# Kernel tuning notes

Measured on AMD Instinct MI355X. Metric: run time of the kernel, lower is better.

The kernel has to match this reference:

```python
import jax, jax.numpy as jnp
import numpy as np

N_HOS, N_TYP, N_STRUCTS = 2, 3, 8
N_COMBOS = N_HOS * N_TYP  # 6
BATCH = 32768
N_ITERS = 150  # PDHG iterations to solve the per-sample QP

S_NP = np.array([[1,0,0,1,0,1,0,0],
                 [0,1,0,1,0,0,1,0],
                 [0,0,1,0,1,0,0,1],
                 [1,0,0,0,1,1,0,0],
                 [0,1,0,0,0,0,1,1],
                 [0,0,1,1,1,0,0,0]], dtype=np.float32)


def setup_inputs() -> dict:
    key = jax.random.key(0)
    ks = jax.random.split(key, 10)
    def lin(kw, fan_in, fan_out):
        lim = 1.0 / np.sqrt(fan_in)
        kw1, kw2 = jax.random.split(kw)
        W = jax.random.uniform(kw1, (fan_out, fan_in), jnp.float32, -lim, lim)
        b = jax.random.uniform(kw2, (fan_out,), jnp.float32, -lim, lim)
        return W, b
    W1, b1 = lin(ks[0], 6, 20)
    W2, b2 = lin(ks[1], 20, 20)
    W3, b3 = lin(ks[2], 20, 20)
    W4, b4 = lin(ks[3], 20, 8)
    X = jax.random.uniform(ks[4], (BATCH, N_HOS, N_TYP), jnp.float32)  # nonneg bids -> feasible QP (x=0)
    return {"X": X, "W1": W1, "b1": b1, "W2": W2, "b2": b2, "W3": W3, "b3": b3,
            "W4": W4, "b4": b4, "S": jnp.asarray(S_NP), "batch_size": BATCH}


def _solve_qp(z, b, S):
    """Batched PDHG for: max w.x - ||x-z||_2  s.t. x>=0, S x <= b, with w = 1.
    z: [B, ns], b: [B, m], S: [m, ns]. Returns x: [B, ns]."""
    B, ns = z.shape
    m = S.shape[0]
    w = jnp.ones_like(z)
    # K = [S; -I]; Frobenius bound on spectral norm (safe step sizes)
    L = jnp.sqrt(jnp.sum(S * S) + ns)
    tau = 0.9 / L
    sigma = 0.9 / L

    def prox_f(u):
        # prox of tau*(||x-z|| - w.x) at u  (closed form: shifted norm shrinkage)
        v = u + tau * w - z
        nv = jnp.linalg.norm(v, axis=-1, keepdims=True)
        scale = jnp.maximum(1.0 - tau / jnp.maximum(nv, 1e-12), 0.0)
        return z + scale * v

    def step(carry, _):
        x, l1, l2 = carry
        x_new = prox_f(x - tau * (l1 @ S - l2))  # K^T lam = S^T l1 - l2
        xbar = 2.0 * x_new - x
        l1n = jnp.maximum(l1 + sigma * (xbar @ S.T) - sigma * b, 0.0)  # dual of Sx<=b
        l2n = jnp.maximum(l2 - sigma * xbar, 0.0)                      # dual of -x<=0
        return (x_new, l1n, l2n), None

    x0 = jnp.maximum(z, 0.0)
    l1 = jnp.zeros((B, m), z.dtype)
    l2 = jnp.zeros((B, ns), z.dtype)
    (x, _, _), _ = jax.lax.scan(step, (x0, l1, l2), None, length=N_ITERS)
    return x


def reference(X, W1, b1, W2, b2, W3, b3, W4, b4, S, batch_size):
    B = X.shape[0]
    Z = X.reshape(B, -1)                       # [B, 6] = bids flattened (also the QP rhs b)
    h = jnp.tanh(Z @ W1.T + b1)
    h = jnp.tanh(h @ W2.T + b2)
    h = jnp.tanh(h @ W3.T + b3)
    z = jnp.tanh(h @ W4.T + b4)                # [B, 8] anchor point for QP
    return _solve_qp(z, Z, S)                  # [B, 8] allocation
```

## Files before the change

### kernel.cpp

```cpp
#include <hip/hip_runtime.h>
#include <math.h>


#define NITERS 150

__device__ __forceinline__ float ftanh(float a) {
    float e = __expf(2.0f * a);
    return fmaf(-2.0f, __builtin_amdgcn_rcpf(e + 1.0f), 1.0f);
}

template<int CTRL>
__device__ __forceinline__ float dpp_add(float x) {
    int xi = __builtin_bit_cast(int, x);
    int yi = __builtin_amdgcn_update_dpp(0, xi, CTRL, 0xF, 0xF, true);
    return x + __builtin_bit_cast(float, yi);
}

__device__ __forceinline__ float bperm(int addr, float v) {
    return __builtin_bit_cast(float,
        __builtin_amdgcn_ds_bpermute(addr, __builtin_bit_cast(int, v)));
}

#define FOR20(M) M(0) M(1) M(2) M(3) M(4) M(5) M(6) M(7) M(8) M(9) \
                 M(10) M(11) M(12) M(13) M(14) M(15) M(16) M(17) M(18) M(19)
#define FOR8(M)  M(0) M(1) M(2) M(3) M(4) M(5) M(6) M(7)

#define DOT20(W, base, H) \
  ( (fmaf(W[(base)+0],H##0,  fmaf(W[(base)+1],H##1,  fmaf(W[(base)+2],H##2,  fmaf(W[(base)+3],H##3,  W[(base)+4]*H##4)))) \
   + fmaf(W[(base)+5],H##5,  fmaf(W[(base)+6],H##6,  fmaf(W[(base)+7],H##7,  fmaf(W[(base)+8],H##8,  W[(base)+9]*H##9))))) \
  + (fmaf(W[(base)+10],H##10, fmaf(W[(base)+11],H##11, fmaf(W[(base)+12],H##12, fmaf(W[(base)+13],H##13, W[(base)+14]*H##14)))) \
   + fmaf(W[(base)+15],H##15, fmaf(W[(base)+16],H##16, fmaf(W[(base)+17],H##17, fmaf(W[(base)+18],H##18, W[(base)+19]*H##19))))) )

#define DOT6(W, base, P) \
  ( fmaf(W[(base)+0],P##0, fmaf(W[(base)+1],P##1, W[(base)+2]*P##2)) \
  + fmaf(W[(base)+3],P##3, fmaf(W[(base)+4],P##4, W[(base)+5]*P##5)) )

__global__ __launch_bounds__(256, 4)
void matchnet_kernel(
    const float* __restrict__ X,
    const float* __restrict__ W1, const float* __restrict__ b1,
    const float* __restrict__ W2, const float* __restrict__ b2,
    const float* __restrict__ W3, const float* __restrict__ b3,
    const float* __restrict__ W4, const float* __restrict__ b4,
    float* __restrict__ out, int B)
{
    const int tid = blockIdx.x * 256 + threadIdx.x;
    const int s   = tid >> 3;
    if (s >= B) return;
    const int g   = tid & 7;

    const float TAU = 0.9f / sqrtf(26.0f);
    const float SIG = TAU;
    const float TS  = TAU * SIG;

    float zin0, zin1, zin2, zin3, zin4, zin5;
    {
        const float2* xp = (const float2*)(X + (size_t)s * 6);
        float2 p0 = xp[0], p1 = xp[1], p2 = xp[2];
        zin0 = p0.x; zin1 = p0.y; zin2 = p1.x;
        zin3 = p1.y; zin4 = p2.x; zin5 = p2.y;
    }

#define L1ROW(j) float h1_##j = ftanh(b1[j] + DOT6(W1, (j)*6, zin));
    FOR20(L1ROW)
#define L2ROW(j) float h2_##j = ftanh(b2[j] + DOT20(W2, (j)*20, h1_));
    FOR20(L2ROW)
#define L3ROW(j) float h3_##j = ftanh(b3[j] + DOT20(W3, (j)*20, h2_));
    FOR20(L3ROW)
#define ZROW(j)  float z##j  = ftanh(b4[j] + DOT20(W4, (j)*20, h3_));
    FOR8(ZROW)

    const bool gb0 = (g & 1), gb1 = (g & 2), gb2 = (g & 4);
    float z01 = gb0 ? z1 : z0;
    float z23 = gb0 ? z3 : z2;
    float z45 = gb0 ? z5 : z4;
    float z67 = gb0 ? z7 : z6;
    float z03 = gb1 ? z23 : z01;
    float z47 = gb1 ? z67 : z45;
    float zg  = gb2 ? z47 : z03;

    float i01 = gb0 ? zin1 : zin0;
    float i23 = gb0 ? zin3 : zin2;
    float i45 = gb0 ? zin5 : zin4;
    float i03 = gb1 ? i23 : i01;
    float ig  = gb2 ? i45 : i03;

    float zpt = zg + TAU;
    float xz  = fmaxf(zg, 0.0f) - zg + TAU;
    float q   = 0.0f;
    float p   = xz;
    float l1  = 0.0f;
    float sb  = SIG * ig;

    const int wl  = threadIdx.x & 63;
    const int gbase = wl & 56;
    const int nib = g * 4;
    const int aStA = (gbase + ((0x21020210u >> nib) & 7)) << 2;
    const int aStB = (gbase + ((0x44331543u >> nib) & 7)) << 2;
    const int aStC = (gbase + ((0x00055000u >> nib) & 7)) << 2;
    const int aRA  = (gbase + ((0x00210210u >> nib) & 7)) << 2;
    const int aRB  = (gbase + ((0x00364433u >> nib) & 7)) << 2;
    const int aRC  = (gbase + ((0x00475765u >> nib) & 7)) << 2;
    const float cm = (g == 3 || g == 4) ? 1.0f : 0.0f;

#pragma unroll 1
    for (int it = 0; it < NITERS; ++it) {
        float s1 = bperm(aStA, l1);
        float s2 = bperm(aStB, l1);
        float s3 = bperm(aStC, l1);
        float st = fmaf(cm, s3, s1 + s2);

        float v = fmaf(-TAU, st, p);

        float nv = v * v;
        nv = dpp_add<0xB1>(nv);
        nv = dpp_add<0x4E>(nv);
        nv = dpp_add<0x141>(nv);

        float scale = fmaxf(fmaf(-TAU, __builtin_amdgcn_rsqf(nv), 1.0f), 0.0f);

        float xb = fmaf(scale + scale, v, zpt - xz);
        xz = fmaf(scale, v, TAU);
        q  = fmaxf(fmaf(-TS, xb, q), 0.0f);
        p  = xz + q;

        float r1 = bperm(aRA, xb);
        float r2 = bperm(aRB, xb);
        float r3 = bperm(aRC, xb);
        float r  = (r1 + r2) + r3;

        l1 = fmaxf(fmaf(SIG, r, l1) - sb, 0.0f);
    }

    out[tid] = xz + zg - TAU;
}

extern "C" void kernel_launch(void* const* d_in, const int* in_sizes, int n_in,
                              void* d_out, int out_size, void* d_ws, size_t ws_size,
                              hipStream_t stream) {
    const float* X  = (const float*)d_in[0];
    const float* W1 = (const float*)d_in[1];
    const float* b1 = (const float*)d_in[2];
    const float* W2 = (const float*)d_in[3];
    const float* b2 = (const float*)d_in[4];
    const float* W3 = (const float*)d_in[5];
    const float* b3 = (const float*)d_in[6];
    const float* W4 = (const float*)d_in[7];
    const float* b4 = (const float*)d_in[8];
    float* out = (float*)d_out;
    const int B = in_sizes[0] / 6;
    const int threads = B * 8;
    const int blocks = (threads + 255) / 256;
    hipLaunchKernelGGL(matchnet_kernel, dim3(blocks), dim3(256), 0, stream,
                       X, W1, b1, W2, b2, W3, b3, W4, b4, out, B);
}
```

Measured before the change: 131.5 us.

## Map each sample to four lanes and replace bpermute gathers with quad-perm DPP

Each sample now uses 4 lanes, each holding two primal and two dual components, instead of 8 lanes with one each. The S and S^T products become quad_perm DPP moves plus selects instead of LDS bpermute gathers, and the norm reduction needs only two DPP steps. This halves the thread count so the redundant MLP prologue is computed half as often, and it removes LDS traffic from the iteration loop. The cost is more ALU work per lane and a lower occupancy hint in launch bounds.

```diff
diff --git a/kernel.cpp b/kernel.cpp
--- a/kernel.cpp
+++ b/kernel.cpp
@@ -9,16 +9,12 @@
     return fmaf(-2.0f, __builtin_amdgcn_rcpf(e + 1.0f), 1.0f);
 }
 
-template<int CTRL>
-__device__ __forceinline__ float dpp_add(float x) {
+template<int P0, int P1, int P2, int P3>
+__device__ __forceinline__ float qp(float x) {
+    constexpr int ctrl = P0 | (P1 << 2) | (P2 << 4) | (P3 << 6);
     int xi = __builtin_bit_cast(int, x);
-    int yi = __builtin_amdgcn_update_dpp(0, xi, CTRL, 0xF, 0xF, true);
-    return x + __builtin_bit_cast(float, yi);
-}
-
-__device__ __forceinline__ float bperm(int addr, float v) {
-    return __builtin_bit_cast(float,
-        __builtin_amdgcn_ds_bpermute(addr, __builtin_bit_cast(int, v)));
+    int yi = __builtin_amdgcn_update_dpp(0, xi, ctrl, 0xF, 0xF, true);
+    return __builtin_bit_cast(float, yi);
 }
 
 #define FOR20(M) M(0) M(1) M(2) M(3) M(4) M(5) M(6) M(7) M(8) M(9) \
@@ -35,7 +31,7 @@
   ( fmaf(W[(base)+0],P##0, fmaf(W[(base)+1],P##1, W[(base)+2]*P##2)) \
   + fmaf(W[(base)+3],P##3, fmaf(W[(base)+4],P##4, W[(base)+5]*P##5)) )
 
-__global__ __launch_bounds__(256, 4)
+__global__ __launch_bounds__(256, 2)
 void matchnet_kernel(
     const float* __restrict__ X,
     const float* __restrict__ W1, const float* __restrict__ b1,
@@ -45,9 +41,9 @@
     float* __restrict__ out, int B)
 {
     const int tid = blockIdx.x * 256 + threadIdx.x;
-    const int s   = tid >> 3;
+    const int s   = tid >> 2;
     if (s >= B) return;
-    const int g   = tid & 7;
+    const int g   = tid & 3;
 
     const float TAU = 0.9f / sqrtf(26.0f);
     const float SIG = TAU;
@@ -70,69 +66,82 @@
 #define ZROW(j)  float z##j  = ftanh(b4[j] + DOT20(W4, (j)*20, h3_));
     FOR8(ZROW)
 
-    const bool gb0 = (g & 1), gb1 = (g & 2), gb2 = (g & 4);
-    float z01 = gb0 ? z1 : z0;
-    float z23 = gb0 ? z3 : z2;
-    float z45 = gb0 ? z5 : z4;
-    float z67 = gb0 ? z7 : z6;
-    float z03 = gb1 ? z23 : z01;
-    float z47 = gb1 ? z67 : z45;
-    float zg  = gb2 ? z47 : z03;
+    const bool b0 = (g & 1), b1_ = (g & 2);
+    float z01 = b0 ? z1 : z0,  z23 = b0 ? z3 : z2;
+    float zA  = b1_ ? z23 : z01;
+    float z45 = b0 ? z5 : z4,  z67 = b0 ? z7 : z6;
+    float zB  = b1_ ? z67 : z45;
 
-    float i01 = gb0 ? zin1 : zin0;
-    float i23 = gb0 ? zin3 : zin2;
-    float i45 = gb0 ? zin5 : zin4;
-    float i03 = gb1 ? i23 : i01;
-    float ig  = gb2 ? i45 : i03;
+    float i01 = b0 ? zin1 : zin0, i23 = b0 ? zin3 : zin2;
+    float igA = b1_ ? i23 : i01;
+    float i45 = b0 ? zin5 : zin4;
+    float sbA = SIG * igA;
+    float sbB = (g < 2) ? SIG * i45 : 1e30f;
 
-    float zpt = zg + TAU;
-    float xz  = fmaxf(zg, 0.0f) - zg + TAU;
-    float q   = 0.0f;
-    float p   = xz;
-    float l1  = 0.0f;
-    float sb  = SIG * ig;
+    float zptA = zA + TAU, zptB = zB + TAU;
+    float xzA  = fmaxf(zA, 0.0f) - zA + TAU;
+    float xzB  = fmaxf(zB, 0.0f) - zB + TAU;
+    float qA = 0.0f, qB = 0.0f;
+    float pA = xzA,  pB = xzB;
+    float lA = 0.0f, lB = 0.0f;
 
-    const int wl  = threadIdx.x & 63;
-    const int gbase = wl & 56;
-    const int nib = g * 4;
-    const int aStA = (gbase + ((0x21020210u >> nib) & 7)) << 2;
-    const int aStB = (gbase + ((0x44331543u >> nib) & 7)) << 2;
-    const int aStC = (gbase + ((0x00055000u >> nib) & 7)) << 2;
-    const int aRA  = (gbase + ((0x00210210u >> nib) & 7)) << 2;
-    const int aRB  = (gbase + ((0x00364433u >> nib) & 7)) << 2;
-    const int aRC  = (gbase + ((0x00475765u >> nib) & 7)) << 2;
-    const float cm = (g == 3 || g == 4) ? 1.0f : 0.0f;
+    const bool sel03 = (g == 0) || (g == 3);
+    const bool sel01 = (g < 2);
+    const bool sel1  = (g == 1);
 
 #pragma unroll 1
     for (int it = 0; it < NITERS; ++it) {
-        float s1 = bperm(aStA, l1);
-        float s2 = bperm(aStB, l1);
-        float s3 = bperm(aStC, l1);
-        float st = fmaf(cm, s3, s1 + s2);
+        float gA1  = qp<0,1,2,0>(lA);
+        float gA2a = qp<3,0,0,1>(lA);
+        float gA2b = qp<0,0,1,0>(lB);
+        float gA2  = sel03 ? gA2a : gA2b;
+        float gA3  = qp<2,2,2,1>(lB);
+        float stA = (gA1 + gA2) + gA3;
+        float gB1  = qp<2,0,1,2>(lA);
+        float gB2a = qp<3,3,0,0>(lA);
+        float gB2b = qp<0,0,0,0>(lB);
+        float gB2  = sel01 ? gB2a : gB2b;
+        float gB3  = qp<1,2,2,2>(lB);
+        float stB = (gB1 + gB2) + gB3;
 
-        float v = fmaf(-TAU, st, p);
+        float vA = fmaf(-TAU, stA, pA);
+        float vB = fmaf(-TAU, stB, pB);
 
-        float nv = v * v;
-        nv = dpp_add<0xB1>(nv);
-        nv = dpp_add<0x4E>(nv);
-        nv = dpp_add<0x141>(nv);
+        float nl = fmaf(vA, vA, vB * vB);
+        nl = nl + qp<1,0,3,2>(nl);
+        nl = nl + qp<2,3,0,1>(nl);
+        float scale = fmaxf(fmaf(-TAU, __builtin_amdgcn_rsqf(nl), 1.0f), 0.0f);
+        float ss2 = scale + scale;
 
-        float scale = fmaxf(fmaf(-TAU, __builtin_amdgcn_rsqf(nv), 1.0f), 0.0f);
+        float xbA = fmaf(ss2, vA, zptA - xzA);
+        float xbB = fmaf(ss2, vB, zptB - xzB);
+        xzA = fmaf(scale, vA, TAU);
+        xzB = fmaf(scale, vB, TAU);
+        qA  = fmaxf(fmaf(-TS, xbA, qA), 0.0f);
+        qB  = fmaxf(fmaf(-TS, xbB, qB), 0.0f);
+        pA  = xzA + qA;
+        pB  = xzB + qB;
 
-        float xb = fmaf(scale + scale, v, zpt - xz);
-        xz = fmaf(scale, v, TAU);
-        q  = fmaxf(fmaf(-TS, xb, q), 0.0f);
-        p  = xz + q;
+        float h1  = qp<0,1,2,0>(xbA);
+        float h2a = qp<3,3,0,0>(xbA);
+        float h2b = qp<0,0,0,0>(xbB);
+        float h2  = sel01 ? h2a : h2b;
+        float h3  = qp<1,2,3,1>(xbB);
+        float rA = (h1 + h2) + h3;
+        float k1  = qp<1,2,0,0>(xbA);
+        float k2a = qp<0,3,0,0>(xbA);
+        float k2b = qp<2,0,0,0>(xbB);
+        float k2  = sel1 ? k2a : k2b;
+        float k3  = qp<3,0,0,0>(xbB);
+        float rB = (k1 + k2) + k3;
 
-        float r1 = bperm(aRA, xb);
-        float r2 = bperm(aRB, xb);
-        float r3 = bperm(aRC, xb);
-        float r  = (r1 + r2) + r3;
-
-        l1 = fmaxf(fmaf(SIG, r, l1) - sb, 0.0f);
+        lA = fmaxf(fmaf(SIG, rA, lA) - sbA, 0.0f);
+        lB = fmaxf(fmaf(SIG, rB, lB) - sbB, 0.0f);
     }
 
-    out[tid] = xz + zg - TAU;
+    const float T2 = 2.0f * TAU;
+    out[(size_t)s * 8 + g]     = xzA + zptA - T2;
+    out[(size_t)s * 8 + 4 + g] = xzB + zptB - T2;
 }
 
 extern "C" void kernel_launch(void* const* d_in, const int* in_sizes, int n_in,
@@ -149,7 +158,7 @@
     const float* b4 = (const float*)d_in[8];
     float* out = (float*)d_out;
     const int B = in_sizes[0] / 6;
-    const int threads = B * 8;
+    const int threads = B * 4;
     const int blocks = (threads + 255) / 256;
     hipLaunchKernelGGL(matchnet_kernel, dim3(blocks), dim3(256), 0, stream,
                        X, W1, b1, W2, b2, W3, b3, W4, b4, out, B);
```

After: 114.6 us. 1.15x faster.

## Replace ds_bpermute exchanges with DPP quad permutes via permuted lane mapping

Applied to the files above, without the earlier changes.

Reassigns which primal/dual variable each of the 8 lanes per sample holds so that the S and S^T products in the PDHG loop can be built from DPP quad permutes and row mirrors instead of six ds_bpermute LDS-crossbar operations per iteration. Adds per-lane selects and masks, pads unused dual lanes with a huge bias so they stay zero, and scatters the output through a permutation table. The aim is to cut the latency of the per-iteration data exchange, at the cost of more VALU selects and fragile lane-mapping logic.

```diff
diff --git a/kernel.cpp b/kernel.cpp
--- a/kernel.cpp
+++ b/kernel.cpp
@@ -10,16 +10,16 @@
 }
 
 template<int CTRL>
-__device__ __forceinline__ float dpp_add(float x) {
+__device__ __forceinline__ float dppmov(float x) {
     int xi = __builtin_bit_cast(int, x);
     int yi = __builtin_amdgcn_update_dpp(0, xi, CTRL, 0xF, 0xF, true);
-    return x + __builtin_bit_cast(float, yi);
+    return __builtin_bit_cast(float, yi);
 }
-
-__device__ __forceinline__ float bperm(int addr, float v) {
-    return __builtin_bit_cast(float,
-        __builtin_amdgcn_ds_bpermute(addr, __builtin_bit_cast(int, v)));
+template<int P0, int P1, int P2, int P3>
+__device__ __forceinline__ float qp(float x) {
+    return dppmov<(P0) | ((P1) << 2) | ((P2) << 4) | ((P3) << 6)>(x);
 }
+#define HMIR 0x141
 
 #define FOR20(M) M(0) M(1) M(2) M(3) M(4) M(5) M(6) M(7) M(8) M(9) \
                  M(10) M(11) M(12) M(13) M(14) M(15) M(16) M(17) M(18) M(19)
@@ -47,7 +47,7 @@
     const int tid = blockIdx.x * 256 + threadIdx.x;
     const int s   = tid >> 3;
     if (s >= B) return;
-    const int g   = tid & 7;
+    const int k   = tid & 7;
 
     const float TAU = 0.9f / sqrtf(26.0f);
     const float SIG = TAU;
@@ -70,69 +70,78 @@
 #define ZROW(j)  float z##j  = ftanh(b4[j] + DOT20(W4, (j)*20, h3_));
     FOR8(ZROW)
 
-    const bool gb0 = (g & 1), gb1 = (g & 2), gb2 = (g & 4);
-    float z01 = gb0 ? z1 : z0;
-    float z23 = gb0 ? z3 : z2;
-    float z45 = gb0 ? z5 : z4;
-    float z67 = gb0 ? z7 : z6;
-    float z03 = gb1 ? z23 : z01;
-    float z47 = gb1 ? z67 : z45;
-    float zg  = gb2 ? z47 : z03;
+    const bool lo = (k & 1), mi = (k & 2), hi = (k & 4);
+    float a_  = lo ? z5 : z0;
+    float b_  = lo ? z4 : z3;
+    float c_  = lo ? z6 : z1;
+    float d_  = lo ? z7 : z2;
+    float e_  = mi ? b_ : a_;
+    float f_  = mi ? d_ : c_;
+    float zg  = hi ? f_ : e_;
+    float a2 = lo ? zin1 : zin0;
+    float b2v = lo ? zin3 : zin2;
+    float c2 = lo ? zin4 : zin5;
+    float e2 = mi ? b2v : a2;
+    float sbv = hi ? c2 : e2;
+    float sb = (k >= 6) ? 1e30f : SIG * sbv;
 
-    float i01 = gb0 ? zin1 : zin0;
-    float i23 = gb0 ? zin3 : zin2;
-    float i45 = gb0 ? zin5 : zin4;
-    float i03 = gb1 ? i23 : i01;
-    float ig  = gb2 ? i45 : i03;
+    const bool mA  = (k < 2);
+    const bool mB  = (k < 4);
+    const bool m23 = (k == 2) || (k == 3);
+    const bool m45 = (k == 4) || (k == 5);
+    const bool mE  = (k == 1) || (k == 2) || (k == 4);
+    const bool m5  = (k == 5);
 
     float zpt = zg + TAU;
     float xz  = fmaxf(zg, 0.0f) - zg + TAU;
     float q   = 0.0f;
     float p   = xz;
-    float l1  = 0.0f;
-    float sb  = SIG * ig;
-
-    const int wl  = threadIdx.x & 63;
-    const int gbase = wl & 56;
-    const int nib = g * 4;
-    const int aStA = (gbase + ((0x21020210u >> nib) & 7)) << 2;
-    const int aStB = (gbase + ((0x44331543u >> nib) & 7)) << 2;
-    const int aStC = (gbase + ((0x00055000u >> nib) & 7)) << 2;
-    const int aRA  = (gbase + ((0x00210210u >> nib) & 7)) << 2;
-    const int aRB  = (gbase + ((0x00364433u >> nib) & 7)) << 2;
-    const int aRC  = (gbase + ((0x00475765u >> nib) & 7)) << 2;
-    const float cm = (g == 3 || g == 4) ? 1.0f : 0.0f;
+    float L   = 0.0f;
 
 #pragma unroll 1
     for (int it = 0; it < NITERS; ++it) {
-        float s1 = bperm(aStA, l1);
-        float s2 = bperm(aStB, l1);
-        float s3 = bperm(aStC, l1);
-        float st = fmaf(cm, s3, s1 + s2);
+        float Lx = qp<1,0,3,2>(L);
+        float Qr = L + Lx;
+        float ML = dppmov<HMIR>(L);
+        float A  = qp<0,0,0,2>(L);
+        float Bq = qp<0,0,0,2>(Qr);
+        float C  = qp<2,2,1,1>(ML);
+        float t1 = mA ? A : (mB ? Bq : C);
+        float D1 = qp<3,3,0,1>(L);
+        float D2 = qp<1,1,3,3>(L);
+        float D3 = qp<1,1,3,3>(ML);
+        float t2 = m23 ? D3 : (m45 ? D2 : D1);
+        float st = t1 + t2;
 
         float v = fmaf(-TAU, st, p);
 
-        float nv = v * v;
-        nv = dpp_add<0xB1>(nv);
-        nv = dpp_add<0x4E>(nv);
-        nv = dpp_add<0x141>(nv);
-
-        float scale = fmaxf(fmaf(-TAU, __builtin_amdgcn_rsqf(nv), 1.0f), 0.0f);
+        float nl = v * v;
+        float n1 = qp<1,0,3,2>(nl);  nl += n1;
+        float n2 = qp<2,3,0,1>(nl);  nl += n2;
+        float n3 = dppmov<HMIR>(nl); nl += n3;
+        float scale = fmaxf(fmaf(-TAU, __builtin_amdgcn_rsqf(nl), 1.0f), 0.0f);
 
         float xb = fmaf(scale + scale, v, zpt - xz);
         xz = fmaf(scale, v, TAU);
         q  = fmaxf(fmaf(-TS, xb, q), 0.0f);
         p  = xz + q;
 
-        float r1 = bperm(aRA, xb);
-        float r2 = bperm(aRB, xb);
-        float r3 = bperm(aRC, xb);
-        float r  = (r1 + r2) + r3;
+        float Pxp = qp<1,0,3,2>(xb);
+        float P   = xb + Pxp;
+        float MP  = dppmov<HMIR>(P);
+        float E1  = qp<0,0,0,0>(P);
+        float E2  = qp<0,2,0,0>(MP);
+        float tP  = mE ? E2 : E1;
+        float F1  = qp<2,2,3,3>(xb);
+        float F2  = qp<3,3,3,3>(xb);
+        float tX  = m5 ? F2 : F1;
+        float r   = tP + tX;
 
-        l1 = fmaxf(fmaf(SIG, r, l1) - sb, 0.0f);
+        L = fmaxf(fmaf(SIG, r, L) - sb, 0.0f);
     }
 
-    out[tid] = xz + zg - TAU;
+    const int opos = (int)((0x72614350u >> (4 * k)) & 7u);
+    out[(size_t)s * 8 + opos] = xz + zg - TAU;
 }
 
 extern "C" void kernel_launch(void* const* d_in, const int* in_sizes, int n_in,
```

Measured after the change: 131.7 us. About the same (+0.1%).
